# Optimization experiments

Measured on AMD Instinct MI355X. Metric: run time of the kernel, lower is better.

## Reference

```python
import jax, jax.numpy as jnp
import numpy as np

ABOVE_MAX_DOY_VALUE = 10000
MTF_FOR_HPF = 0.4
MAX_MASKED_RATE = 0.5
UP_FACTOR = 2


def _psf_kernel(c: int, mtf_fc: float) -> jnp.ndarray:
    """Gaussian PSF kernel whose MTF at Nyquist (fc = 0.5/mtf_res) equals mtf_fc.
    mtf_res = res = 1.0 -> half_kernel_width = 1 -> 3x3 kernel, identical per channel."""
    mtf_res = 1.0
    # sigma = sqrt(-ln(mtf_fc)) / (sqrt(2) * pi * fc), fc = 0.5 / mtf_res
    sigma = mtf_res * np.sqrt(-2.0 * np.log(mtf_fc)) / np.pi
    hkw = int(np.ceil(mtf_res / 1.0))  # = 1
    coords = np.arange(-hkw, hkw + 1, dtype=np.float64)
    d2 = coords[:, None] ** 2 + coords[None, :] ** 2
    k = np.exp(-d2 / (2.0 * sigma * sigma))
    k = (k / k.sum()).astype(np.float32)
    return jnp.asarray(np.broadcast_to(k, (c, 1) + k.shape).copy())  # [c,1,3,3]


def setup_inputs() -> dict:
    key = jax.random.key(0)
    k1, k2, k3, k4 = jax.random.split(key, 4)
    lr_data = jax.random.normal(k1, (1, 20, 4, 256, 256), dtype=jnp.float32)
    hr_data = jax.random.normal(k2, (1, 30, 4, 512, 512), dtype=jnp.float32)
    # unique, sorted DOYs; every lr date has >=2 strictly earlier hr dates
    lr_doy = (30 + 16 * jnp.arange(20, dtype=jnp.int32))[None, :]   # 30..334
    hr_doy = (1 + 12 * jnp.arange(30, dtype=jnp.int32))[None, :]    # 1..349
    lr_mask = jax.random.uniform(k3, (1, 20, 256, 256)) < 0.05
    hr_mask = jax.random.uniform(k4, (1, 30, 512, 512)) < 0.08  # rate < 0.5 everywhere
    return {"lr_data": lr_data, "hr_data": hr_data, "lr_doy": lr_doy,
            "hr_doy": hr_doy, "lr_mask": lr_mask, "hr_mask": hr_mask}


def reference(lr_data, hr_data, lr_doy, hr_doy, lr_mask, hr_mask):
    b, t_lr, c, h0, w0 = lr_data.shape
    H, W = h0 * UP_FACTOR, w0 * UP_FACTOR
    t_hr = hr_data.shape[1]

    # DateWiseSITSModule: bilinear upsampling of data, nearest for mask
    lr_up = jax.image.resize(lr_data, (b, t_lr, c, H, W), method="linear")
    lr_mask_up = jax.image.resize(lr_mask.astype(jnp.float32), (b, t_lr, H, W),
                                  method="nearest") > 0.5

    # DOY difference matrix [t_hr, t_lr]; negative (hr after lr) -> ABOVE
    diff = lr_doy[0, None, :] - hr_doy[0, :, None]
    diff = jnp.where(diff < 0, ABOVE_MAX_DOY_VALUE, diff)
    # exclude heavily masked hr frames
    rate = hr_mask.astype(jnp.float32).mean(axis=(-1, -2))[0]  # [t_hr]
    diff = jnp.where((rate > MAX_MASKED_RATE)[:, None], ABOVE_MAX_DOY_VALUE, diff)

    first_min = diff.min(axis=0)
    first_idx = diff.argmin(axis=0)                         # [t_lr]
    first_vals = hr_doy[0, first_idx]                       # [t_lr]
    # mask out the first minimum (vectorized form of the per-column loop)
    diff2 = diff.at[first_idx, jnp.arange(t_lr)].set(ABOVE_MAX_DOY_VALUE)
    second_min = diff2.min(axis=0)
    second_idx = diff2.argmin(axis=0)
    second_vals = hr_doy[0, second_idx]

    valid = (first_min < ABOVE_MAX_DOY_VALUE) & (second_min < ABOVE_MAX_DOY_VALUE)

    masked_first = hr_mask[:, first_idx]                    # [b,t_lr,H,W]
    masked_second = hr_mask[:, second_idx]

    g1 = hr_data[:, first_idx]                              # [b,t_lr,c,H,W]
    g2 = hr_data[:, second_idx]
    fv = first_vals.astype(lr_data.dtype)[None, :, None, None, None]
    sv = second_vals.astype(lr_data.dtype)[None, :, None, None, None]
    coef_a = (g2 - g1) / (sv - fv)
    coef_b = g2 - coef_a * sv
    doy_f = lr_doy.astype(lr_data.dtype)[:, :, None, None, None]
    predicted_hr = coef_a * doy_f + coef_b                  # [b,t_lr,c,H,W]

    # high-pass filter: x - depthwise PSF lowpass
    kernel = _psf_kernel(c, MTF_FOR_HPF)                    # [c,1,3,3]
    x = predicted_hr.reshape(b * t_lr, c, H, W)
    low = jax.lax.conv_general_dilated(x, kernel, (1, 1), "SAME",
                                       feature_group_count=c)
    hpf = (x - low).reshape(b, t_lr, c, H, W)

    final_mask = (lr_mask_up
                  | (~valid)[None, :, None, None]
                  | masked_first
                  | masked_second)
    final_hr = lr_up + hpf
    return final_hr, final_mask, lr_up
```

## Files before the change

kernel.cpp:

```cpp
#include <hip/hip_runtime.h>
#include <math.h>

#define T_LR 20
#define T_HR 30
#define CCH  4
#define H0   256
#define W0   256
#define HH   512
#define WW   512
#define ABOVE 10000

typedef float f32x4 __attribute__((ext_vector_type(4)));

#define WS_FIDX  0
#define WS_SIDX  32
#define WS_ALPHA 64
#define WS_BETA  96
#define WS_VALID 128
#define WS_CNT   160

__global__ void rate_kernel(const int* __restrict__ hr_mask,
                            int* __restrict__ wsi) {
    int j = blockIdx.x >> 4;
    int slice = blockIdx.x & 15;
    const int elems = HH * WW / 16;
    const uint4* p = (const uint4*)(hr_mask + (size_t)j * HH * WW + (size_t)slice * elems);
    int sum = 0;
    for (int e = threadIdx.x; e < elems / 4; e += blockDim.x) {
        uint4 v = p[e];
        sum += (int)(v.x + v.y + v.z + v.w);
    }
    for (int o = 32; o; o >>= 1) sum += __shfl_down(sum, o);
    __shared__ int ssum[4];
    if ((threadIdx.x & 63) == 0) ssum[threadIdx.x >> 6] = sum;
    __syncthreads();
    if (threadIdx.x == 0)
        wsi[WS_CNT + blockIdx.x] = ssum[0] + ssum[1] + ssum[2] + ssum[3];
}

__global__ void select_kernel(const int* __restrict__ lr_doy,
                              const int* __restrict__ hr_doy,
                              float* __restrict__ ws) {
    __shared__ int masked[T_HR];
    __shared__ int hdoy[T_HR];
    const int* wsi_c = (const int*)ws;
    int tid = threadIdx.x;
    if (tid < T_HR) {
        int cnt = 0;
        #pragma unroll
        for (int k = 0; k < 16; k++) cnt += wsi_c[WS_CNT + 16 * tid + k];
        masked[tid] = (float)cnt / (float)(HH * WW) > 0.5f;
        hdoy[tid] = hr_doy[tid];
    }
    __syncthreads();
    int i = tid;
    if (i >= T_LR) return;
    int doy = lr_doy[i];

    int fmin = ABOVE, fidx = 0;
    #pragma unroll
    for (int j = 0; j < T_HR; j++) {
        int d = doy - hdoy[j];
        if (d < 0) d = ABOVE;
        if (masked[j]) d = ABOVE;
        if (d < fmin) { fmin = d; fidx = j; }
    }
    int smin = ABOVE, sidx = 0;
    #pragma unroll
    for (int j = 0; j < T_HR; j++) {
        int d = doy - hdoy[j];
        if (d < 0) d = ABOVE;
        if (masked[j]) d = ABOVE;
        if (j == fidx) d = ABOVE;
        if (d < smin) { smin = d; sidx = j; }
    }
    int valid = (fmin < ABOVE) && (smin < ABOVE);
    float fv = (float)hdoy[fidx], sv = (float)hdoy[sidx];
    float denom = sv - fv;

    int* wsi = (int*)ws;
    wsi[WS_FIDX + i] = fidx;
    wsi[WS_SIDX + i] = sidx;
    ws[WS_ALPHA + i] = (sv - (float)doy) / denom;
    ws[WS_BETA + i]  = ((float)doy - fv) / denom;
    wsi[WS_VALID + i] = valid;
}

__launch_bounds__(256)
__global__ void fuse_kernel(const float* __restrict__ lr_data,
                            const float* __restrict__ hr_data,
                            const int* __restrict__ lr_mask,
                            const int* __restrict__ hr_mask,
                            const float* __restrict__ ws,
                            float* __restrict__ out,
                            float ga, float gb) {
    const int lin = blockIdx.x + (blockIdx.y << 4) + (blockIdx.z << 8);
    const int q = lin >> 3;
    const int z = (lin & 7) * 10 + (q >> 8);
    const int t = q & 255;
    const int i  = z >> 2;
    const int ch = z & 3;
    const int x0 = (t & 15) * 32;
    const int y0 = (t >> 4) * 32;
    const int tid = threadIdx.x;
    const int ty = tid >> 3, tx4 = tid & 7;
    const int y = y0 + ty, x = x0 + tx4 * 4;

    const int* wsi = (const int*)ws;
    const int f       = wsi[WS_FIDX + i];
    const int s       = wsi[WS_SIDX + i];
    const float alpha = ws[WS_ALPHA + i];
    const float beta  = ws[WS_BETA + i];
    const int valid   = wsi[WS_VALID + i];

    __shared__ float Hs[2][34][36];
    __shared__ float hxs[18][36];

    const float* g0 = hr_data + ((size_t)f * CCH + ch) * HH * WW;
    const float* g1 = hr_data + ((size_t)s * CCH + ch) * HH * WW;

    f32x4 xc0, xc1;
    {
        const float* gp = g0 + (size_t)y * WW;
        f32x4 v = *(const f32x4*)(gp + x);
        xc0 = v;
        float xl = (x > 0)      ? gp[x - 1] : 0.f;
        float xr = (x + 4 < WW) ? gp[x + 4] : 0.f;
        f32x4 H;
        H.x = ga * (xl  + v.y) + gb * v.x;
        H.y = ga * (v.x + v.z) + gb * v.y;
        H.z = ga * (v.y + v.w) + gb * v.z;
        H.w = ga * (v.z + xr ) + gb * v.w;
        *(f32x4*)&Hs[0][ty + 1][tx4 * 4] = H;
    }
    {
        const float* gp = g1 + (size_t)y * WW;
        f32x4 v = *(const f32x4*)(gp + x);
        xc1 = v;
        float xl = (x > 0)      ? gp[x - 1] : 0.f;
        float xr = (x + 4 < WW) ? gp[x + 4] : 0.f;
        f32x4 H;
        H.x = ga * (xl  + v.y) + gb * v.x;
        H.y = ga * (v.x + v.z) + gb * v.y;
        H.z = ga * (v.y + v.w) + gb * v.z;
        H.w = ga * (v.z + xr ) + gb * v.w;
        *(f32x4*)&Hs[1][ty + 1][tx4 * 4] = H;
    }

    if (tid < 32) {
        int img  = tid >> 4;
        int top  = (tid >> 3) & 1;
        int quad = tid & 7;
        int rr = top ? 33 : 0;
        int gy = y0 - 1 + rr;
        f32x4 H = {0.f, 0.f, 0.f, 0.f};
        if (gy >= 0 && gy < HH) {
            const float* gp = (img ? g1 : g0) + (size_t)gy * WW;
            int gx = x0 + quad * 4;
            f32x4 v = *(const f32x4*)(gp + gx);
            float xl = (gx > 0)      ? gp[gx - 1] : 0.f;
            float xr = (gx + 4 < WW) ? gp[gx + 4] : 0.f;
            H.x = ga * (xl  + v.y) + gb * v.x;
            H.y = ga * (v.x + v.z) + gb * v.y;
            H.z = ga * (v.y + v.w) + gb * v.z;
            H.w = ga * (v.z + xr ) + gb * v.w;
        }
        *(f32x4*)&Hs[img][rr][quad * 4] = H;
    }

    const int ly0 = (y0 >> 1) - 1;
    if (tid < 144) {
        int r = tid >> 3, tq = tid & 7;
        int gy = min(max(ly0 + r, 0), H0 - 1);
        const float* lp = lr_data + ((size_t)i * CCH + ch) * H0 * W0 + (size_t)gy * W0;
        int J = (x0 >> 1) + tq * 2;
        float vm = lp[max(J - 1, 0)];
        float v0 = lp[J];
        float v1 = lp[J + 1];
        float v2 = lp[min(J + 2, W0 - 1)];
        f32x4 hx;
        hx.x = 0.75f * v0 + 0.25f * vm;
        hx.y = 0.75f * v0 + 0.25f * v1;
        hx.z = 0.75f * v1 + 0.25f * v0;
        hx.w = 0.75f * v1 + 0.25f * v2;
        *(f32x4*)&hxs[r][tq * 4] = hx;
    }

    const int jy = y >> 1;
    int4 mf = make_int4(0, 0, 0, 0), ms = make_int4(0, 0, 0, 0);
    int m0 = 0, m1 = 0;
    if (ch == 0) {
        mf = *(const int4*)(hr_mask + ((size_t)f * HH + y) * WW + x);
        ms = *(const int4*)(hr_mask + ((size_t)s * HH + y) * WW + x);
        const int* lm = lr_mask + ((size_t)i * H0 + jy) * W0;
        m0 = lm[x >> 1];
        m1 = lm[(x >> 1) + 1];
    }
    __syncthreads();

    const int c = tx4 * 4;
    f32x4 hu0 = *(const f32x4*)&Hs[0][ty    ][c];
    f32x4 hm0 = *(const f32x4*)&Hs[0][ty + 1][c];
    f32x4 hd0 = *(const f32x4*)&Hs[0][ty + 2][c];
    f32x4 hu1 = *(const f32x4*)&Hs[1][ty    ][c];
    f32x4 hm1 = *(const f32x4*)&Hs[1][ty + 1][c];
    f32x4 hd1 = *(const f32x4*)&Hs[1][ty + 2][c];
    f32x4 hp0 = xc0 - (ga * (hu0 + hd0) + gb * hm0);
    f32x4 hp1 = xc1 - (ga * (hu1 + hd1) + gb * hm1);

    const int rc = jy - ly0;
    const int rn = jy + ((y & 1) ? 1 : -1) - ly0;
    f32x4 ha = *(const f32x4*)&hxs[rc][c];
    f32x4 hb = *(const f32x4*)&hxs[rn][c];
    f32x4 lu = 0.75f * ha + 0.25f * hb;

    const size_t outM  = (size_t)T_LR * CCH * HH * WW;
    const size_t outLU = outM + (size_t)T_LR * HH * WW;
    const size_t oidx = (((size_t)i * CCH + ch) * HH + y) * WW + x;

    f32x4 fh = lu + alpha * hp0 + beta * hp1;
    __builtin_nontemporal_store(fh, (f32x4*)&out[oidx]);
    __builtin_nontemporal_store(lu, (f32x4*)&out[outLU + oidx]);

    if (ch == 0) {
        int nv = !valid;
        f32x4 mo;
        mo.x = (m0 | mf.x | ms.x | nv) ? 1.f : 0.f;
        mo.y = (m0 | mf.y | ms.y | nv) ? 1.f : 0.f;
        mo.z = (m1 | mf.z | ms.z | nv) ? 1.f : 0.f;
        mo.w = (m1 | mf.w | ms.w | nv) ? 1.f : 0.f;
        __builtin_nontemporal_store(mo, (f32x4*)&out[outM + ((size_t)i * HH + y) * WW + x]);
    }
}

extern "C" void kernel_launch(void* const* d_in, const int* in_sizes, int n_in,
                              void* d_out, int out_size, void* d_ws, size_t ws_size,
                              hipStream_t stream) {
    const float* lr_data = (const float*)d_in[0];
    const float* hr_data = (const float*)d_in[1];
    const int* lr_doy    = (const int*)d_in[2];
    const int* hr_doy    = (const int*)d_in[3];
    const int* lr_mask   = (const int*)d_in[4];
    const int* hr_mask   = (const int*)d_in[5];
    float* out = (float*)d_out;
    float* ws  = (float*)d_ws;
    int* wsi   = (int*)d_ws;

    double sigma = sqrt(-2.0 * log(0.4)) / M_PI;
    double e1 = exp(-1.0 / (2.0 * sigma * sigma));
    double axis_sum = 1.0 + 2.0 * e1;
    float ga = (float)(e1 / axis_sum);
    float gb = (float)(1.0 / axis_sum);

    rate_kernel<<<T_HR * 16, 256, 0, stream>>>(hr_mask, wsi);
    select_kernel<<<1, 64, 0, stream>>>(lr_doy, hr_doy, ws);

    dim3 grid(WW / 32, HH / 32, T_LR * CCH);
    fuse_kernel<<<grid, 256, 0, stream>>>(lr_data, hr_data, lr_mask, hr_mask,
                                          ws, out, ga, gb);
}
```

Measured before the change: 74.66 us.

## Make fuse kernel persistent with register-prefetched software pipeline over tiles

Turns the fuse kernel into a semi-persistent kernel: each of 2048 blocks processes 10 consecutive tiles. The global loads for the next tile are issued into registers before the current tile is computed, then written to shared memory after a barrier. The aim is to hide global-load latency and cut block launch overhead. In exchange it adds extra barriers per tile, raises register pressure, and leaves fewer blocks in flight to hide latency.

```diff
diff --git a/kernel.cpp b/kernel.cpp
--- a/kernel.cpp
+++ b/kernel.cpp
@@ -86,6 +86,8 @@
     wsi[WS_VALID + i] = valid;
 }
 
+#define TPB 10
+
 __launch_bounds__(256)
 __global__ void fuse_kernel(const float* __restrict__ lr_data,
                             const float* __restrict__ hr_data,
@@ -94,142 +96,181 @@
                             const float* __restrict__ ws,
                             float* __restrict__ out,
                             float ga, float gb) {
-    const int lin = blockIdx.x + (blockIdx.y << 4) + (blockIdx.z << 8);
-    const int q = lin >> 3;
-    const int z = (lin & 7) * 10 + (q >> 8);
-    const int t = q & 255;
-    const int i  = z >> 2;
-    const int ch = z & 3;
-    const int x0 = (t & 15) * 32;
-    const int y0 = (t >> 4) * 32;
+    const int b = blockIdx.x;
+    const int tile0 = (b & 7) * (TPB * 256) + (b >> 3) * TPB;
     const int tid = threadIdx.x;
     const int ty = tid >> 3, tx4 = tid & 7;
-    const int y = y0 + ty, x = x0 + tx4 * 4;
+    const int cq = tx4 * 4;
 
     const int* wsi = (const int*)ws;
-    const int f       = wsi[WS_FIDX + i];
-    const int s       = wsi[WS_SIDX + i];
-    const float alpha = ws[WS_ALPHA + i];
-    const float beta  = ws[WS_BETA + i];
-    const int valid   = wsi[WS_VALID + i];
 
     __shared__ float Hs[2][34][36];
     __shared__ float hxs[18][36];
 
-    const float* g0 = hr_data + ((size_t)f * CCH + ch) * HH * WW;
-    const float* g1 = hr_data + ((size_t)s * CCH + ch) * HH * WW;
-
+    f32x4 nx0, nx1;
+    float nxl0, nxr0, nxl1, nxr1;
+    f32x4 ne; float nel, ner;
+    float nvm, nv0, nv1, nv2;
     f32x4 xc0, xc1;
-    {
-        const float* gp = g0 + (size_t)y * WW;
-        f32x4 v = *(const f32x4*)(gp + x);
-        xc0 = v;
-        float xl = (x > 0)      ? gp[x - 1] : 0.f;
-        float xr = (x + 4 < WW) ? gp[x + 4] : 0.f;
-        f32x4 H;
-        H.x = ga * (xl  + v.y) + gb * v.x;
-        H.y = ga * (v.x + v.z) + gb * v.y;
-        H.z = ga * (v.y + v.w) + gb * v.z;
-        H.w = ga * (v.z + xr ) + gb * v.w;
-        *(f32x4*)&Hs[0][ty + 1][tx4 * 4] = H;
-    }
-    {
-        const float* gp = g1 + (size_t)y * WW;
-        f32x4 v = *(const f32x4*)(gp + x);
-        xc1 = v;
-        float xl = (x > 0)      ? gp[x - 1] : 0.f;
-        float xr = (x + 4 < WW) ? gp[x + 4] : 0.f;
-        f32x4 H;
-        H.x = ga * (xl  + v.y) + gb * v.x;
-        H.y = ga * (v.x + v.z) + gb * v.y;
-        H.z = ga * (v.y + v.w) + gb * v.z;
-        H.w = ga * (v.z + xr ) + gb * v.w;
-        *(f32x4*)&Hs[1][ty + 1][tx4 * 4] = H;
-    }
-
-    if (tid < 32) {
-        int img  = tid >> 4;
-        int top  = (tid >> 3) & 1;
-        int quad = tid & 7;
-        int rr = top ? 33 : 0;
-        int gy = y0 - 1 + rr;
-        f32x4 H = {0.f, 0.f, 0.f, 0.f};
-        if (gy >= 0 && gy < HH) {
-            const float* gp = (img ? g1 : g0) + (size_t)gy * WW;
-            int gx = x0 + quad * 4;
-            f32x4 v = *(const f32x4*)(gp + gx);
-            float xl = (gx > 0)      ? gp[gx - 1] : 0.f;
-            float xr = (gx + 4 < WW) ? gp[gx + 4] : 0.f;
-            H.x = ga * (xl  + v.y) + gb * v.x;
-            H.y = ga * (v.x + v.z) + gb * v.y;
-            H.z = ga * (v.y + v.w) + gb * v.z;
-            H.w = ga * (v.z + xr ) + gb * v.w;
-        }
-        *(f32x4*)&Hs[img][rr][quad * 4] = H;
-    }
-
-    const int ly0 = (y0 >> 1) - 1;
-    if (tid < 144) {
-        int r = tid >> 3, tq = tid & 7;
-        int gy = min(max(ly0 + r, 0), H0 - 1);
-        const float* lp = lr_data + ((size_t)i * CCH + ch) * H0 * W0 + (size_t)gy * W0;
-        int J = (x0 >> 1) + tq * 2;
-        float vm = lp[max(J - 1, 0)];
-        float v0 = lp[J];
-        float v1 = lp[J + 1];
-        float v2 = lp[min(J + 2, W0 - 1)];
-        f32x4 hx;
-        hx.x = 0.75f * v0 + 0.25f * vm;
-        hx.y = 0.75f * v0 + 0.25f * v1;
-        hx.z = 0.75f * v1 + 0.25f * v0;
-        hx.w = 0.75f * v1 + 0.25f * v2;
-        *(f32x4*)&hxs[r][tq * 4] = hx;
-    }
-
-    const int jy = y >> 1;
-    int4 mf = make_int4(0, 0, 0, 0), ms = make_int4(0, 0, 0, 0);
-    int m0 = 0, m1 = 0;
-    if (ch == 0) {
-        mf = *(const int4*)(hr_mask + ((size_t)f * HH + y) * WW + x);
-        ms = *(const int4*)(hr_mask + ((size_t)s * HH + y) * WW + x);
-        const int* lm = lr_mask + ((size_t)i * H0 + jy) * W0;
-        m0 = lm[x >> 1];
-        m1 = lm[(x >> 1) + 1];
-    }
+
+    auto load_tile = [&](int tile) {
+        int z = tile >> 8, t = tile & 255;
+        int x0 = (t & 15) * 32, y0 = (t >> 4) * 32;
+        int i = z >> 2, ch = z & 3;
+        int f = wsi[WS_FIDX + i], s = wsi[WS_SIDX + i];
+        const float* g0 = hr_data + ((size_t)f * CCH + ch) * HH * WW;
+        const float* g1 = hr_data + ((size_t)s * CCH + ch) * HH * WW;
+        int y = y0 + ty, x = x0 + cq;
+        {
+            const float* gp = g0 + (size_t)y * WW;
+            nx0  = *(const f32x4*)(gp + x);
+            nxl0 = (x > 0)      ? gp[x - 1] : 0.f;
+            nxr0 = (x + 4 < WW) ? gp[x + 4] : 0.f;
+        }
+        {
+            const float* gp = g1 + (size_t)y * WW;
+            nx1  = *(const f32x4*)(gp + x);
+            nxl1 = (x > 0)      ? gp[x - 1] : 0.f;
+            nxr1 = (x + 4 < WW) ? gp[x + 4] : 0.f;
+        }
+        if (tid < 32) {
+            int img  = tid >> 4;
+            int top  = (tid >> 3) & 1;
+            int quad = tid & 7;
+            int gy = y0 - 1 + (top ? 33 : 0);
+            ne = f32x4{0.f, 0.f, 0.f, 0.f}; nel = 0.f; ner = 0.f;
+            if (gy >= 0 && gy < HH) {
+                const float* gp = (img ? g1 : g0) + (size_t)gy * WW;
+                int gx = x0 + quad * 4;
+                ne  = *(const f32x4*)(gp + gx);
+                nel = (gx > 0)      ? gp[gx - 1] : 0.f;
+                ner = (gx + 4 < WW) ? gp[gx + 4] : 0.f;
+            }
+        }
+        if (tid >= 112) {
+            int idx = tid - 112;
+            int r = idx >> 3, tq = idx & 7;
+            int ly0 = (y0 >> 1) - 1;
+            int gy = min(max(ly0 + r, 0), H0 - 1);
+            const float* lp = lr_data + ((size_t)i * CCH + ch) * H0 * W0 + (size_t)gy * W0;
+            int J = (x0 >> 1) + tq * 2;
+            nvm = lp[max(J - 1, 0)];
+            nv0 = lp[J];
+            nv1 = lp[J + 1];
+            nv2 = lp[min(J + 2, W0 - 1)];
+        }
+    };
+
+    auto write_tile = [&]() {
+        {
+            f32x4 H;
+            H.x = ga * (nxl0  + nx0.y) + gb * nx0.x;
+            H.y = ga * (nx0.x + nx0.z) + gb * nx0.y;
+            H.z = ga * (nx0.y + nx0.w) + gb * nx0.z;
+            H.w = ga * (nx0.z + nxr0 ) + gb * nx0.w;
+            *(f32x4*)&Hs[0][ty + 1][cq] = H;
+        }
+        {
+            f32x4 H;
+            H.x = ga * (nxl1  + nx1.y) + gb * nx1.x;
+            H.y = ga * (nx1.x + nx1.z) + gb * nx1.y;
+            H.z = ga * (nx1.y + nx1.w) + gb * nx1.z;
+            H.w = ga * (nx1.z + nxr1 ) + gb * nx1.w;
+            *(f32x4*)&Hs[1][ty + 1][cq] = H;
+        }
+        xc0 = nx0; xc1 = nx1;
+        if (tid < 32) {
+            int img  = tid >> 4;
+            int top  = (tid >> 3) & 1;
+            int quad = tid & 7;
+            f32x4 H;
+            H.x = ga * (nel  + ne.y) + gb * ne.x;
+            H.y = ga * (ne.x + ne.z) + gb * ne.y;
+            H.z = ga * (ne.y + ne.w) + gb * ne.z;
+            H.w = ga * (ne.z + ner ) + gb * ne.w;
+            *(f32x4*)&Hs[img][top ? 33 : 0][quad * 4] = H;
+        }
+        if (tid >= 112) {
+            int idx = tid - 112;
+            int r = idx >> 3, tq = idx & 7;
+            f32x4 hx;
+            hx.x = 0.75f * nv0 + 0.25f * nvm;
+            hx.y = 0.75f * nv0 + 0.25f * nv1;
+            hx.z = 0.75f * nv1 + 0.25f * nv0;
+            hx.w = 0.75f * nv1 + 0.25f * nv2;
+            *(f32x4*)&hxs[r][tq * 4] = hx;
+        }
+    };
+
+    auto compute_tile = [&](int tile) {
+        int z = tile >> 8, t = tile & 255;
+        int x0 = (t & 15) * 32, y0 = (t >> 4) * 32;
+        int i = z >> 2, ch = z & 3;
+        int y = y0 + ty, x = x0 + cq;
+        int jy = y >> 1;
+
+        int4 mf = make_int4(0, 0, 0, 0), ms = make_int4(0, 0, 0, 0);
+        int m0 = 0, m1 = 0;
+        if (ch == 0) {
+            int f = wsi[WS_FIDX + i], s = wsi[WS_SIDX + i];
+            mf = *(const int4*)(hr_mask + ((size_t)f * HH + y) * WW + x);
+            ms = *(const int4*)(hr_mask + ((size_t)s * HH + y) * WW + x);
+            const int* lm = lr_mask + ((size_t)i * H0 + jy) * W0;
+            m0 = lm[x >> 1];
+            m1 = lm[(x >> 1) + 1];
+        }
+        const float alpha = ws[WS_ALPHA + i];
+        const float beta  = ws[WS_BETA + i];
+        const int valid   = wsi[WS_VALID + i];
+
+        f32x4 hu0 = *(const f32x4*)&Hs[0][ty    ][cq];
+        f32x4 hm0 = *(const f32x4*)&Hs[0][ty + 1][cq];
+        f32x4 hd0 = *(const f32x4*)&Hs[0][ty + 2][cq];
+        f32x4 hu1 = *(const f32x4*)&Hs[1][ty    ][cq];
+        f32x4 hm1 = *(const f32x4*)&Hs[1][ty + 1][cq];
+        f32x4 hd1 = *(const f32x4*)&Hs[1][ty + 2][cq];
+        f32x4 hp0 = xc0 - (ga * (hu0 + hd0) + gb * hm0);
+        f32x4 hp1 = xc1 - (ga * (hu1 + hd1) + gb * hm1);
+
+        int ly0 = (y0 >> 1) - 1;
+        int rc = jy - ly0;
+        int rn = jy + ((y & 1) ? 1 : -1) - ly0;
+        f32x4 ha = *(const f32x4*)&hxs[rc][cq];
+        f32x4 hb = *(const f32x4*)&hxs[rn][cq];
+        f32x4 lu = 0.75f * ha + 0.25f * hb;
+
+        const size_t outM  = (size_t)T_LR * CCH * HH * WW;
+        const size_t outLU = outM + (size_t)T_LR * HH * WW;
+        const size_t oidx = (((size_t)i * CCH + ch) * HH + y) * WW + x;
+
+        f32x4 fh = lu + alpha * hp0 + beta * hp1;
+        __builtin_nontemporal_store(fh, (f32x4*)&out[oidx]);
+        __builtin_nontemporal_store(lu, (f32x4*)&out[outLU + oidx]);
+
+        if (ch == 0) {
+            int nv = !valid;
+            f32x4 mo;
+            mo.x = (m0 | mf.x | ms.x | nv) ? 1.f : 0.f;
+            mo.y = (m0 | mf.y | ms.y | nv) ? 1.f : 0.f;
+            mo.z = (m1 | mf.z | ms.z | nv) ? 1.f : 0.f;
+            mo.w = (m1 | mf.w | ms.w | nv) ? 1.f : 0.f;
+            __builtin_nontemporal_store(mo, (f32x4*)&out[outM + ((size_t)i * HH + y) * WW + x]);
+        }
+    };
+
+    load_tile(tile0);
+    write_tile();
     __syncthreads();
 
-    const int c = tx4 * 4;
-    f32x4 hu0 = *(const f32x4*)&Hs[0][ty    ][c];
-    f32x4 hm0 = *(const f32x4*)&Hs[0][ty + 1][c];
-    f32x4 hd0 = *(const f32x4*)&Hs[0][ty + 2][c];
-    f32x4 hu1 = *(const f32x4*)&Hs[1][ty    ][c];
-    f32x4 hm1 = *(const f32x4*)&Hs[1][ty + 1][c];
-    f32x4 hd1 = *(const f32x4*)&Hs[1][ty + 2][c];
-    f32x4 hp0 = xc0 - (ga * (hu0 + hd0) + gb * hm0);
-    f32x4 hp1 = xc1 - (ga * (hu1 + hd1) + gb * hm1);
-
-    const int rc = jy - ly0;
-    const int rn = jy + ((y & 1) ? 1 : -1) - ly0;
-    f32x4 ha = *(const f32x4*)&hxs[rc][c];
-    f32x4 hb = *(const f32x4*)&hxs[rn][c];
-    f32x4 lu = 0.75f * ha + 0.25f * hb;
-
-    const size_t outM  = (size_t)T_LR * CCH * HH * WW;
-    const size_t outLU = outM + (size_t)T_LR * HH * WW;
-    const size_t oidx = (((size_t)i * CCH + ch) * HH + y) * WW + x;
-
-    f32x4 fh = lu + alpha * hp0 + beta * hp1;
-    __builtin_nontemporal_store(fh, (f32x4*)&out[oidx]);
-    __builtin_nontemporal_store(lu, (f32x4*)&out[outLU + oidx]);
-
-    if (ch == 0) {
-        int nv = !valid;
-        f32x4 mo;
-        mo.x = (m0 | mf.x | ms.x | nv) ? 1.f : 0.f;
-        mo.y = (m0 | mf.y | ms.y | nv) ? 1.f : 0.f;
-        mo.z = (m1 | mf.z | ms.z | nv) ? 1.f : 0.f;
-        mo.w = (m1 | mf.w | ms.w | nv) ? 1.f : 0.f;
-        __builtin_nontemporal_store(mo, (f32x4*)&out[outM + ((size_t)i * HH + y) * WW + x]);
+    #pragma unroll 1
+    for (int k = 0; k < TPB; ++k) {
+        if (k < TPB - 1) load_tile(tile0 + k + 1);
+        compute_tile(tile0 + k);
+        __syncthreads();
+        if (k < TPB - 1) {
+            write_tile();
+            __syncthreads();
+        }
     }
 }
 
@@ -255,7 +296,6 @@
     rate_kernel<<<T_HR * 16, 256, 0, stream>>>(hr_mask, wsi);
     select_kernel<<<1, 64, 0, stream>>>(lr_doy, hr_doy, ws);
 
-    dim3 grid(WW / 32, HH / 32, T_LR * CCH);
-    fuse_kernel<<<grid, 256, 0, stream>>>(lr_data, hr_data, lr_mask, hr_mask,
+    fuse_kernel<<<2048, 256, 0, stream>>>(lr_data, hr_data, lr_mask, hr_mask,
                                           ws, out, ga, gb);
 }
```

New measurement: 104.3 us. 39.7% more time.
